# Kernel optimization log

Measured on AMD Instinct MI355X. Metric: run time of the kernel, lower is better.

## Reference

```python
import jax, jax.numpy as jnp
import numpy as np

COST_CLASS = 1.0
COST_POLYLINE = 1.0
COST_DIRECTION = 1.0
EPS = 1e-6


def setup_inputs() -> dict:
    key = jax.random.key(0)
    k1, k2, k3, k4 = jax.random.split(key, 4)
    bs, Q, C, P, T = 2, 256, 16, 20, 256
    return {
        "pred_logits": jax.random.normal(k1, (bs, Q, C), dtype=jnp.float32),
        "pred_polylines": jax.random.normal(k2, (bs, Q, P, 2), dtype=jnp.float32),
        "tgt_labels": jax.random.randint(k3, (T,), 0, C),
        "tgt_polylines": jax.random.normal(k4, (T, P, 2), dtype=jnp.float32),
    }


def reference(pred_logits, pred_polylines, tgt_labels, tgt_polylines):
    # pred_logits: [bs, Q, C]; pred_polylines: [bs, Q, P, 2]
    # tgt_labels: [T]; tgt_polylines: [T, P, 2]
    bs, Q = pred_logits.shape[:2]
    out_prob = jax.nn.softmax(pred_logits.reshape(bs * Q, -1), axis=-1)  # [N, C]
    out_poly = pred_polylines.reshape(bs * Q, *pred_polylines.shape[2:])  # [N, P, 2]

    # classification cost: -p(tgt_class)  -> [N, T]
    cost_class = -out_prob[:, tgt_labels]

    # pairwise polyline L1 cdist, all pairs at once: d[n, t, p, q]
    d = (jnp.abs(out_poly[:, None, :, None, 0] - tgt_polylines[None, :, None, :, 0])
         + jnp.abs(out_poly[:, None, :, None, 1] - tgt_polylines[None, :, None, :, 1]))
    # bidirectional average-of-min distance (Chamfer-style), averaged -> [N, T]
    min1 = d.min(axis=3).mean(axis=2)  # pred -> gt
    min2 = d.min(axis=2).mean(axis=2)  # gt -> pred
    cost_polyline = (min1 + min2) / 2

    # direction cost: 1 - cos(start->end vectors)
    pd = out_poly[:, -1] - out_poly[:, 0]          # [N, 2]
    gd = tgt_polylines[:, -1] - tgt_polylines[:, 0]  # [T, 2]
    pd = pd / (jnp.linalg.norm(pd, axis=-1, keepdims=True) + EPS)
    gd = gd / (jnp.linalg.norm(gd, axis=-1, keepdims=True) + EPS)
    cost_direction = 1.0 - pd @ gd.T               # [N, T]

    C = (COST_CLASS * cost_class
         + COST_POLYLINE * cost_polyline
         + COST_DIRECTION * cost_direction)
    return C.reshape(bs, Q, -1)
```

## Files before the change

kernel.cpp:

```cpp
#include <hip/hip_runtime.h>
#include <math.h>

#define BS    2
#define NQ    256
#define NCLS  16
#define NP    20
#define NT    256
#define NN    (BS * NQ)
#define FEPS  1e-6f
#define QPL   5
#define TPB   64
#define PHALF 10
#define THREADS 256

__global__ __launch_bounds__(THREADS, 8) void matcher_cost_kernel(
    const float* __restrict__ logits,
    const float* __restrict__ ppoly,
    const int*   __restrict__ tlabels,
    const float* __restrict__ tpoly,
    float*       __restrict__ out)
{
    const int bid   = blockIdx.x;
    const int n     = bid >> 2;
    const int tbase = (bid & 3) * TPB;
    const int tid   = threadIdx.x;
    const int t     = tbase + (tid >> 2);
    const int z     = tid & 3;

    __shared__ float2 s_pxy[NP];
    __shared__ float  s_logit[NCLS];
    __shared__ float  s_prob[NCLS];
    __shared__ float  s_dir[2];
    __shared__ float  s_invden;

    if (tid < NP * 2) ((float*)s_pxy)[tid] = ppoly[n * NP * 2 + tid];
    if (tid < NCLS)   s_logit[tid] = logits[n * NCLS + tid];
    __syncthreads();

    if (tid < NCLS) {
        float mx = s_logit[0];
        #pragma unroll
        for (int c = 1; c < NCLS; ++c) mx = fmaxf(mx, s_logit[c]);
        s_prob[tid] = __expf(s_logit[tid] - mx);
    }
    if (tid == 0) {
        float den = 0.f;
        #pragma unroll
        for (int c = 0; c < NCLS; ++c) den += s_prob[c];
        s_invden = 1.f / den;
    }
    if (tid == 16) {
        float2 a = s_pxy[0], b = s_pxy[NP - 1];
        float dx = b.x - a.x, dy = b.y - a.y;
        float nrm = sqrtf(dx * dx + dy * dy) + FEPS;
        s_dir[0] = dx / nrm; s_dir[1] = dy / nrm;
    }

    float tx[QPL], ty[QPL], m2[QPL];
    const float* tp = &tpoly[(t * NP + z * QPL) * 2];
    #pragma unroll
    for (int k = 0; k < QPL; ++k) {
        float2 v = *reinterpret_cast<const float2*>(&tp[2 * k]);
        tx[k] = v.x; ty[k] = v.y; m2[k] = 1e30f;
    }

    float sum1 = 0.f;
    float m1a[PHALF];
    #pragma unroll
    for (int h = 0; h < 2; ++h) {
        #pragma unroll
        for (int pp = 0; pp < PHALF; ++pp) {
            const float2 pxy = s_pxy[h * PHALF + pp];
            const float d0 = fabsf(pxy.x - tx[0]) + fabsf(pxy.y - ty[0]);
            const float d1 = fabsf(pxy.x - tx[1]) + fabsf(pxy.y - ty[1]);
            const float d2 = fabsf(pxy.x - tx[2]) + fabsf(pxy.y - ty[2]);
            const float d3 = fabsf(pxy.x - tx[3]) + fabsf(pxy.y - ty[3]);
            const float d4 = fabsf(pxy.x - tx[4]) + fabsf(pxy.y - ty[4]);
            m2[0] = fminf(m2[0], d0);
            m2[1] = fminf(m2[1], d1);
            m2[2] = fminf(m2[2], d2);
            m2[3] = fminf(m2[3], d3);
            m2[4] = fminf(m2[4], d4);
            m1a[pp] = fminf(fminf(fminf(d0, d1), d2), fminf(d3, d4));
        }
        float s = 0.f;
        #pragma unroll
        for (int pp = 0; pp < PHALF; ++pp) {
            float v = m1a[pp];
            v = fminf(v, __shfl_xor(v, 1));
            v = fminf(v, __shfl_xor(v, 2));
            s += v;
        }
        sum1 += s;
    }
    float sum2 = ((m2[0] + m2[1]) + (m2[2] + m2[3])) + m2[4];
    sum2 += __shfl_xor(sum2, 1);
    sum2 += __shfl_xor(sum2, 2);
    const float cost_poly = (sum1 + sum2) * (0.5f / (float)NP);

    const float g0x = __shfl(tx[0], 0, 4);
    const float g0y = __shfl(ty[0], 0, 4);
    const float g1x = __shfl(tx[QPL - 1], 3, 4);
    const float g1y = __shfl(ty[QPL - 1], 3, 4);

    __syncthreads();

    if (z == 0) {
        const int lbl = tlabels[t];
        const float cost_class = -s_prob[lbl] * s_invden;

        const float gdx = g1x - g0x, gdy = g1y - g0y;
        const float gn = sqrtf(gdx * gdx + gdy * gdy) + FEPS;
        const float cost_dir = 1.f - (s_dir[0] * gdx + s_dir[1] * gdy) / gn;

        out[n * NT + t] = cost_class + cost_poly + cost_dir;
    }
}

extern "C" void kernel_launch(void* const* d_in, const int* in_sizes, int n_in,
                              void* d_out, int out_size, void* d_ws, size_t ws_size,
                              hipStream_t stream) {
    const float* logits  = (const float*)d_in[0];
    const float* ppoly   = (const float*)d_in[1];
    const int*   tlabels = (const int*)d_in[2];
    const float* tpoly   = (const float*)d_in[3];
    float*       out     = (float*)d_out;

    matcher_cost_kernel<<<dim3(NN * (NT / TPB)), dim3(THREADS), 0, stream>>>(
        logits, ppoly, tlabels, tpoly, out);
}
```

Before: 13.45 us.

## Drop shared memory and barriers; load pred polyline and logits into registers per thread

Removes the shared-memory staging of the predicted polyline, logits, softmax and direction vector, along with both __syncthreads barriers. Each thread now reads the 20 predicted points and 16 logits straight from global memory (uniform per block, so they should hit cache), and the z==0 lanes compute the softmax and the direction normalisation themselves. It also vectorises the target polyline load into float4s and relaxes launch bounds. The trade is more redundant global loads and register pressure per thread, plus duplicated softmax work across lanes.

After: 14.67 us. +9.1%, slower.

```diff
diff --git a/kernel.cpp b/kernel.cpp
--- a/kernel.cpp
+++ b/kernel.cpp
@@ -13,7 +13,7 @@
 #define PHALF 10
 #define THREADS 256
 
-__global__ __launch_bounds__(THREADS, 8) void matcher_cost_kernel(
+__global__ __launch_bounds__(THREADS) void matcher_cost_kernel(
     const float* __restrict__ logits,
     const float* __restrict__ ppoly,
     const int*   __restrict__ tlabels,
@@ -27,91 +27,89 @@
     const int t     = tbase + (tid >> 2);
     const int z     = tid & 3;
 
-    __shared__ float2 s_pxy[NP];
-    __shared__ float  s_logit[NCLS];
-    __shared__ float  s_prob[NCLS];
-    __shared__ float  s_dir[2];
-    __shared__ float  s_invden;
+    float px[NP], py[NP];
+    const float* pp = ppoly + n * NP * 2;
+    #pragma unroll
+    for (int p = 0; p < NP; ++p) { px[p] = pp[2 * p]; py[p] = pp[2 * p + 1]; }
 
-    if (tid < NP * 2) ((float*)s_pxy)[tid] = ppoly[n * NP * 2 + tid];
-    if (tid < NCLS)   s_logit[tid] = logits[n * NCLS + tid];
-    __syncthreads();
-
-    if (tid < NCLS) {
-        float mx = s_logit[0];
-        #pragma unroll
-        for (int c = 1; c < NCLS; ++c) mx = fmaxf(mx, s_logit[c]);
-        s_prob[tid] = __expf(s_logit[tid] - mx);
-    }
-    if (tid == 0) {
-        float den = 0.f;
-        #pragma unroll
-        for (int c = 0; c < NCLS; ++c) den += s_prob[c];
-        s_invden = 1.f / den;
-    }
-    if (tid == 16) {
-        float2 a = s_pxy[0], b = s_pxy[NP - 1];
-        float dx = b.x - a.x, dy = b.y - a.y;
-        float nrm = sqrtf(dx * dx + dy * dy) + FEPS;
-        s_dir[0] = dx / nrm; s_dir[1] = dy / nrm;
-    }
+    float lg[NCLS];
+    const float* lp = logits + n * NCLS;
+    #pragma unroll
+    for (int c = 0; c < NCLS; ++c) lg[c] = lp[c];
 
     float tx[QPL], ty[QPL], m2[QPL];
-    const float* tp = &tpoly[(t * NP + z * QPL) * 2];
-    #pragma unroll
-    for (int k = 0; k < QPL; ++k) {
-        float2 v = *reinterpret_cast<const float2*>(&tp[2 * k]);
-        tx[k] = v.x; ty[k] = v.y; m2[k] = 1e30f;
+    {
+        const float* tp = &tpoly[(t * NP + z * QPL) * 2];
+        float4 a = *reinterpret_cast<const float4*>(tp);
+        float4 b = *reinterpret_cast<const float4*>(tp + 4);
+        float2 c = *reinterpret_cast<const float2*>(tp + 8);
+        tx[0] = a.x; ty[0] = a.y; tx[1] = a.z; ty[1] = a.w;
+        tx[2] = b.x; ty[2] = b.y; tx[3] = b.z; ty[3] = b.w;
+        tx[4] = c.x; ty[4] = c.y;
+        #pragma unroll
+        for (int k = 0; k < QPL; ++k) m2[k] = 1e30f;
     }
 
     float sum1 = 0.f;
-    float m1a[PHALF];
     #pragma unroll
     for (int h = 0; h < 2; ++h) {
+        float m1a[PHALF];
         #pragma unroll
-        for (int pp = 0; pp < PHALF; ++pp) {
-            const float2 pxy = s_pxy[h * PHALF + pp];
-            const float d0 = fabsf(pxy.x - tx[0]) + fabsf(pxy.y - ty[0]);
-            const float d1 = fabsf(pxy.x - tx[1]) + fabsf(pxy.y - ty[1]);
-            const float d2 = fabsf(pxy.x - tx[2]) + fabsf(pxy.y - ty[2]);
-            const float d3 = fabsf(pxy.x - tx[3]) + fabsf(pxy.y - ty[3]);
-            const float d4 = fabsf(pxy.x - tx[4]) + fabsf(pxy.y - ty[4]);
+        for (int pp2 = 0; pp2 < PHALF; ++pp2) {
+            const int p = h * PHALF + pp2;
+            const float vx = px[p];
+            const float vy = py[p];
+            const float d0 = fabsf(vx - tx[0]) + fabsf(vy - ty[0]);
+            const float d1 = fabsf(vx - tx[1]) + fabsf(vy - ty[1]);
+            const float d2 = fabsf(vx - tx[2]) + fabsf(vy - ty[2]);
+            const float d3 = fabsf(vx - tx[3]) + fabsf(vy - ty[3]);
+            const float d4 = fabsf(vx - tx[4]) + fabsf(vy - ty[4]);
             m2[0] = fminf(m2[0], d0);
             m2[1] = fminf(m2[1], d1);
             m2[2] = fminf(m2[2], d2);
             m2[3] = fminf(m2[3], d3);
             m2[4] = fminf(m2[4], d4);
-            m1a[pp] = fminf(fminf(fminf(d0, d1), d2), fminf(d3, d4));
+            m1a[pp2] = fminf(fminf(fminf(d0, d1), d2), fminf(d3, d4));
         }
         float s = 0.f;
         #pragma unroll
-        for (int pp = 0; pp < PHALF; ++pp) {
-            float v = m1a[pp];
-            v = fminf(v, __shfl_xor(v, 1));
-            v = fminf(v, __shfl_xor(v, 2));
+        for (int pp2 = 0; pp2 < PHALF; ++pp2) {
+            float v = m1a[pp2];
+            v = fminf(v, __shfl_xor(v, 1, 4));
+            v = fminf(v, __shfl_xor(v, 2, 4));
             s += v;
         }
         sum1 += s;
     }
     float sum2 = ((m2[0] + m2[1]) + (m2[2] + m2[3])) + m2[4];
-    sum2 += __shfl_xor(sum2, 1);
-    sum2 += __shfl_xor(sum2, 2);
+    sum2 += __shfl_xor(sum2, 1, 4);
+    sum2 += __shfl_xor(sum2, 2, 4);
     const float cost_poly = (sum1 + sum2) * (0.5f / (float)NP);
 
-    const float g0x = __shfl(tx[0], 0, 4);
-    const float g0y = __shfl(ty[0], 0, 4);
-    const float g1x = __shfl(tx[QPL - 1], 3, 4);
-    const float g1y = __shfl(ty[QPL - 1], 3, 4);
-
-    __syncthreads();
+    const float g1x = __shfl_xor(tx[QPL - 1], 3, 4);
+    const float g1y = __shfl_xor(ty[QPL - 1], 3, 4);
 
     if (z == 0) {
+        float mx = lg[0];
+        #pragma unroll
+        for (int c = 1; c < NCLS; ++c) mx = fmaxf(mx, lg[c]);
+        float den = 0.f, pl = 0.f;
         const int lbl = tlabels[t];
-        const float cost_class = -s_prob[lbl] * s_invden;
+        #pragma unroll
+        for (int c = 0; c < NCLS; ++c) {
+            const float e = __expf(lg[c] - mx);
+            den += e;
+            if (c == lbl) pl = e;
+        }
+        const float cost_class = -pl / den;
 
-        const float gdx = g1x - g0x, gdy = g1y - g0y;
+        float pdx = px[NP - 1] - px[0];
+        float pdy = py[NP - 1] - py[0];
+        const float pn = sqrtf(pdx * pdx + pdy * pdy) + FEPS;
+        const float gdx = g1x - tx[0];
+        const float gdy = g1y - ty[0];
         const float gn = sqrtf(gdx * gdx + gdy * gdy) + FEPS;
-        const float cost_dir = 1.f - (s_dir[0] * gdx + s_dir[1] * gdy) / gn;
+        const float cost_dir = 1.f - (pdx * gdx + pdy * gdy) / (pn * gn);
 
         out[n * NT + t] = cost_class + cost_poly + cost_dir;
     }
```
